# Kernel optimization log

Hardware: AMD Instinct MI355X
Metric: run time of the kernel (lower is better)

The kernel has to match this reference:

```python
import jax, jax.numpy as jnp
import numpy as np

N_NODES = 50000
N_EDGES = 800000
IN_CH = 128
EDGE_DIM = 16
N_GRAPHS = 500


def _lin_params(key, din, dout):
    k1, k2 = jax.random.split(key)
    s = 1.0 / np.sqrt(din)
    W = jax.random.uniform(k1, (din, dout), jnp.float32, -s, s)
    b = jax.random.uniform(k2, (dout,), jnp.float32, -s, s)
    return W, b


def setup_inputs() -> dict:
    key = jax.random.key(0)
    ks = jax.random.split(key, 20)
    x = jax.random.normal(ks[0], (N_NODES, IN_CH), jnp.float32)
    edge_attr = jax.random.normal(ks[1], (N_EDGES, EDGE_DIM), jnp.float32)
    edge_index = jax.random.randint(ks[2], (2, N_EDGES), 0, N_NODES, jnp.int32)
    n_nodes = jnp.full((N_GRAPHS,), N_NODES // N_GRAPHS, jnp.int32)
    inp = {"x": x, "edge_attr": edge_attr, "edge_index": edge_index, "n_nodes": n_nodes}
    # conv1: edge lin (edge_dim->128), mlp 128->256->256, bn 256
    inp["We1"], inp["be1"] = _lin_params(ks[3], EDGE_DIM, IN_CH)
    inp["W11"], inp["b11"] = _lin_params(ks[4], IN_CH, 256)
    inp["W12"], inp["b12"] = _lin_params(ks[5], 256, 256)
    inp["g1"], inp["bt1"] = jnp.ones((256,), jnp.float32), jnp.zeros((256,), jnp.float32)
    # conv2: edge lin (edge_dim->256), mlp 256->128->128, bn 128
    inp["We2"], inp["be2"] = _lin_params(ks[6], EDGE_DIM, 256)
    inp["W21"], inp["b21"] = _lin_params(ks[7], 256, 128)
    inp["W22"], inp["b22"] = _lin_params(ks[8], 128, 128)
    inp["g2"], inp["bt2"] = jnp.ones((128,), jnp.float32), jnp.zeros((128,), jnp.float32)
    # conv3: edge lin (edge_dim->128), mlp 128->64->64, bn 64
    inp["We3"], inp["be3"] = _lin_params(ks[9], EDGE_DIM, 128)
    inp["W31"], inp["b31"] = _lin_params(ks[10], 128, 64)
    inp["W32"], inp["b32"] = _lin_params(ks[11], 64, 64)
    inp["g3"], inp["bt3"] = jnp.ones((64,), jnp.float32), jnp.zeros((64,), jnp.float32)
    # head
    inp["Wf1"], inp["bf1"] = _lin_params(ks[12], 64, 16)
    inp["Wf2"], inp["bf2"] = _lin_params(ks[13], 16, 1)
    return inp


def _gine(x, src, dst, ea_proj, W1, b1, W2, b2):
    # message: relu(x_j + lin(edge_attr)); aggregate: scatter-add; GIN0 eps=0
    m = jax.nn.relu(x[src] + ea_proj)                      # [E, D]
    agg = jax.ops.segment_sum(m, dst, num_segments=N_NODES)
    h = x + agg
    return jax.nn.relu(h @ W1 + b1) @ W2 + b2


def _bn(x, g, b):
    mu = x.mean(axis=0)
    var = x.var(axis=0)
    return (x - mu) * jax.lax.rsqrt(var + 1e-5) * g + b


def reference(x, edge_attr, edge_index, n_nodes,
              We1, be1, W11, b11, W12, b12, g1, bt1,
              We2, be2, W21, b21, W22, b22, g2, bt2,
              We3, be3, W31, b31, W32, b32, g3, bt3,
              Wf1, bf1, Wf2, bf2):
    src, dst = edge_index[0], edge_index[1]
    h = _gine(x, src, dst, edge_attr @ We1 + be1, W11, b11, W12, b12)
    h = _bn(jax.nn.relu(h), g1, bt1)
    h = _gine(h, src, dst, edge_attr @ We2 + be2, W21, b21, W22, b22)
    h = _bn(jax.nn.relu(h), g2, bt2)
    h = _gine(h, src, dst, edge_attr @ We3 + be3, W31, b31, W32, b32)
    h = _bn(jax.nn.relu(h), g3, bt3)
    last_idx = jnp.cumsum(n_nodes) - 1                      # [G]
    master = h[last_idx]                                    # [G, 64]; dropout = identity (eval)
    out = jax.nn.relu(master @ Wf1 + bf1) @ Wf2 + bf2       # [G, 1]
    return out
```

## Files before the change

### kernel.cpp

```cpp
#include <hip/hip_runtime.h>
#include <hip/hip_bf16.h>


typedef __attribute__((ext_vector_type(8))) short short8;
typedef __attribute__((ext_vector_type(4))) float floatx4;
typedef __attribute__((ext_vector_type(2))) float float2v;
typedef unsigned long long u64;

__device__ __forceinline__ float2v splat2(float s) {
    float2v v; v[0] = s; v[1] = s; return v;
}

__device__ __forceinline__ int uni(int x) {
    return __builtin_amdgcn_readfirstlane(x);
}

__device__ __forceinline__ float2v pkfma_lo(u64 s, float2v w, float2v p) {
    asm("v_pk_fma_f32 %0, %1, %2, %0 op_sel:[0,0,0] op_sel_hi:[0,1,1]"
        : "+v"(p) : "s"(s), "v"(w));
    return p;
}

__device__ __forceinline__ float2v pkfma_hi(u64 s, float2v w, float2v p) {
    asm("v_pk_fma_f32 %0, %1, %2, %0 op_sel:[1,0,0] op_sel_hi:[1,1,1]"
        : "+v"(p) : "s"(s), "v"(w));
    return p;
}

__device__ __forceinline__ ushort f2bf_rne(float x) {
    unsigned u = __float_as_uint(x);
    unsigned r = (u + 0x7FFFu + ((u >> 16) & 1u)) >> 16;
    return (ushort)r;
}

__device__ __forceinline__ float bf2f(ushort u) {
    return __uint_as_float(((unsigned)u) << 16);
}


__global__ __launch_bounds__(256) void hist_kernel(const int* __restrict__ dst,
                                                   int* __restrict__ deg, int E) {
    int i = blockIdx.x * blockDim.x + threadIdx.x;
    int stride = gridDim.x * blockDim.x;
    for (; i < E; i += stride) atomicAdd(&deg[dst[i]], 1);
}

__global__ __launch_bounds__(1024) void scan_kernel(const int* __restrict__ deg,
                                                    int* __restrict__ row_start, int N) {
    __shared__ int part[1024];
    int tid = threadIdx.x;
    int per = (N + 1023) / 1024;
    int start = tid * per;
    int end = min(start + per, N);
    int s = 0;
    for (int i = start; i < end; ++i) s += deg[i];
    part[tid] = s;
    __syncthreads();
    if (tid == 0) {
        int t = 0;
        for (int i = 0; i < 1024; ++i) {
            int v = part[i];
            part[i] = t;
            t += v;
        }
    }
    __syncthreads();
    int run = part[tid];
    for (int i = start; i < end; ++i) {
        row_start[i] = run;
        run += deg[i];
    }
    if (tid == 1023) row_start[N] = run;
}

__global__ __launch_bounds__(256) void scatter_kernel(
    const int* __restrict__ src, const int* __restrict__ dst,
    const int* __restrict__ row_start, int* __restrict__ cursor,
    int2* __restrict__ csr, int E) {
    int i = blockIdx.x * blockDim.x + threadIdx.x;
    int stride = gridDim.x * blockDim.x;
    for (; i < E; i += stride) {
        int v = dst[i];
        int p = row_start[v] + atomicAdd(&cursor[v], 1);
        csr[p] = make_int2(i, src[i]);
    }
}

__device__ __forceinline__ void wsplit(const float* W, ushort* Wth, ushort* Wtl,
                                       int K, int N, int t) {
    int k = t / N, n = t - k * N;
    float v = W[t];
    ushort hv = f2bf_rne(v);
    float hf = bf2f(hv);
    ushort lv = f2bf_rne(v - hf);
    Wth[(size_t)n * K + k] = hv;
    Wtl[(size_t)n * K + k] = lv;
}

__global__ __launch_bounds__(256) void prep_all(
    const float* W11, ushort* W11h, ushort* W11l,
    const float* W12, ushort* W12h, ushort* W12l,
    const float* W21, ushort* W21h, ushort* W21l,
    const float* W22, ushort* W22h, ushort* W22l,
    const float* W31, ushort* W31h, ushort* W31l,
    const float* W32, ushort* W32h, ushort* W32l) {
    int t = blockIdx.x * blockDim.x + threadIdx.x;
    const int s1 = 128 * 256, s2 = s1 + 256 * 256, s3 = s2 + 256 * 128;
    const int s4 = s3 + 128 * 128, s5 = s4 + 128 * 64, s6 = s5 + 64 * 64;
    if (t < s1) wsplit(W11, W11h, W11l, 128, 256, t);
    else if (t < s2) wsplit(W12, W12h, W12l, 256, 256, t - s1);
    else if (t < s3) wsplit(W21, W21h, W21l, 256, 128, t - s2);
    else if (t < s4) wsplit(W22, W22h, W22l, 128, 128, t - s3);
    else if (t < s5) wsplit(W31, W31h, W31l, 128, 64, t - s4);
    else if (t < s6) wsplit(W32, W32h, W32l, 64, 64, t - s5);
}

__global__ __launch_bounds__(256) void f32_to_bf16(const float* __restrict__ in,
                                                   ushort* __restrict__ out, long n4) {
    long i = (long)blockIdx.x * blockDim.x + threadIdx.x;
    long stride = (long)gridDim.x * blockDim.x;
    for (; i < n4; i += stride) {
        float4 v = ((const float4*)in)[i];
        ushort4 o;
        o.x = f2bf_rne(v.x);
        o.y = f2bf_rne(v.y);
        o.z = f2bf_rne(v.z);
        o.w = f2bf_rne(v.w);
        ((ushort4*)out)[i] = o;
    }
}

__device__ __forceinline__ float2v edge_accum(
    const float* __restrict__ ea, int eid, unsigned rv,
    const float2v* w, float2v bias, float2v acc, float2v z2) {
    const u64* q = (const u64*)(ea + (size_t)eid * 16);
    float2v p = bias;
#pragma unroll
    for (int t = 0; t < 8; ++t) {
        u64 qt = q[t];
        p = pkfma_lo(qt, w[2 * t], p);
        p = pkfma_hi(qt, w[2 * t + 1], p);
    }
    float2v hv;
    hv[0] = __uint_as_float(rv << 16);
    hv[1] = __uint_as_float(rv & 0xffff0000u);
    float2v m = p + hv;
    return acc + __builtin_elementwise_max(m, z2);
}

template <int D, int WPN>
__global__ __launch_bounds__(256) void gine_agg_kernel(
    const float* __restrict__ h, const ushort* __restrict__ hb,
    const float* __restrict__ ea,
    const int* __restrict__ row_start, const int2* __restrict__ csr,
    const float* __restrict__ We, const float* __restrict__ be,
    ushort* __restrict__ uhi, ushort* __restrict__ ulo, int N) {
    constexpr int NPB = 4 / WPN;
    const int lane = threadIdx.x & 63;
    const int wid = threadIdx.x >> 6;
    const int ch0 = (wid % WPN) * 128 + lane * 2;

    float2v w[16];
#pragma unroll
    for (int k = 0; k < 16; ++k) w[k] = *(const float2v*)&We[k * D + ch0];
    const float2v bias = *(const float2v*)&be[ch0];

    int v = blockIdx.x * NPB + wid / WPN;
    const int vstride = gridDim.x * NPB;
    const float2v z2 = splat2(0.f);

    for (; v < N; v += vstride) {
        const int vs = uni(v);
        const int e0 = uni(row_start[vs]);
        const int e1 = uni(row_start[vs + 1]);
        float2v acc = z2;

        int i = e0;
        int rem = e1 - e0;
        if (rem >= 4) {
            int2 c0 = csr[i], c1 = csr[i + 1], c2 = csr[i + 2], c3 = csr[i + 3];
            do {
                const int ni = (rem >= 8) ? i + 4 : i;
                int2 n0 = csr[ni], n1 = csr[ni + 1];
                int2 n2 = csr[ni + 2], n3 = csr[ni + 3];

                const int sA = uni(c0.y), sB = uni(c1.y);
                const int sC = uni(c2.y), sD = uni(c3.y);
                const int eA = uni(c0.x), eB = uni(c1.x);
                const int eC = uni(c2.x), eD = uni(c3.x);

                unsigned rA = *(const unsigned*)&hb[(size_t)sA * D + ch0];
                unsigned rB = *(const unsigned*)&hb[(size_t)sB * D + ch0];
                unsigned rC = *(const unsigned*)&hb[(size_t)sC * D + ch0];
                unsigned rD = *(const unsigned*)&hb[(size_t)sD * D + ch0];

                acc = edge_accum(ea, eA, rA, w, bias, acc, z2);
                acc = edge_accum(ea, eB, rB, w, bias, acc, z2);
                acc = edge_accum(ea, eC, rC, w, bias, acc, z2);
                acc = edge_accum(ea, eD, rD, w, bias, acc, z2);

                c0 = n0; c1 = n1; c2 = n2; c3 = n3;
                i += 4;
                rem -= 4;
            } while (rem >= 4);
        }
        for (; rem > 0; --rem, ++i) {
            int2 ce = csr[i];
            const int se = uni(ce.y);
            const int ee = uni(ce.x);
            unsigned rv = *(const unsigned*)&hb[(size_t)se * D + ch0];
            acc = edge_accum(ea, ee, rv, w, bias, acc, z2);
        }
        float2v sv = *(const float2v*)&h[(size_t)v * D + ch0];
        float u0 = sv[0] + acc[0];
        float u1 = sv[1] + acc[1];
        ushort h0 = f2bf_rne(u0);
        ushort h1 = f2bf_rne(u1);
        ushort l0 = f2bf_rne(u0 - bf2f(h0));
        ushort l1 = f2bf_rne(u1 - bf2f(h1));
        *(ushort2*)&uhi[(size_t)v * D + ch0] = make_ushort2(h0, h1);
        *(ushort2*)&ulo[(size_t)v * D + ch0] = make_ushort2(l0, l1);
    }
}

template <int WRITE_BF16, int STATS>
__global__ __launch_bounds__(256) void gemm_mfma(
    const ushort* __restrict__ Ah, const ushort* __restrict__ Al,
    const ushort* __restrict__ Bh, const ushort* __restrict__ Bl,
    const float* __restrict__ bias,
    float* __restrict__ Cf, ushort* __restrict__ Chi, ushort* __restrict__ Clo,
    float* __restrict__ stats, int Nreal,
    int N, int K, int relu) {
    __shared__ ushort sA[2][128][72];
    __shared__ ushort sB[2][64][72];
    const int tid = threadIdx.x;
    const int wave = tid >> 6, lane = tid & 63;
    const int lrow = lane & 15, lquad = lane >> 4;
    const int bm = blockIdx.y * 128;
    const int bn = blockIdx.x * 64;

    floatx4 acc[2][4];
#pragma unroll
    for (int i = 0; i < 2; ++i)
#pragma unroll
        for (int j = 0; j < 4; ++j) acc[i][j] = (floatx4)0.f;

    for (int k0 = 0; k0 < K; k0 += 64) {
        for (int s = tid; s < 1024; s += 256) {
            int row = s >> 3, c8 = (s & 7) * 8;
            size_t g = (size_t)(bm + row) * K + k0 + c8;
            *(int4*)&sA[0][row][c8] = *(const int4*)&Ah[g];
            *(int4*)&sA[1][row][c8] = *(const int4*)&Al[g];
        }
        for (int s = tid; s < 512; s += 256) {
            int row = s >> 3, c8 = (s & 7) * 8;
            size_t g = (size_t)(bn + row) * K + k0 + c8;
            *(int4*)&sB[0][row][c8] = *(const int4*)&Bh[g];
            *(int4*)&sB[1][row][c8] = *(const int4*)&Bl[g];
        }
        __syncthreads();
        const int rb = wave * 32;
#pragma unroll
        for (int kk = 0; kk < 2; ++kk) {
            int ko = kk * 32 + lquad * 8;
            short8 ah[2], al[2], bh[4], bl[4];
#pragma unroll
            for (int i = 0; i < 2; ++i) {
                ah[i] = *(const short8*)&sA[0][rb + i * 16 + lrow][ko];
                al[i] = *(const short8*)&sA[1][rb + i * 16 + lrow][ko];
            }
#pragma unroll
            for (int j = 0; j < 4; ++j) {
                bh[j] = *(const short8*)&sB[0][j * 16 + lrow][ko];
                bl[j] = *(const short8*)&sB[1][j * 16 + lrow][ko];
            }
#pragma unroll
            for (int i = 0; i < 2; ++i)
#pragma unroll
                for (int j = 0; j < 4; ++j) {
                    acc[i][j] = __builtin_amdgcn_mfma_f32_16x16x32_bf16(
                        ah[i], bh[j], acc[i][j], 0, 0, 0);
                    acc[i][j] = __builtin_amdgcn_mfma_f32_16x16x32_bf16(
                        ah[i], bl[j], acc[i][j], 0, 0, 0);
                    acc[i][j] = __builtin_amdgcn_mfma_f32_16x16x32_bf16(
                        al[i], bh[j], acc[i][j], 0, 0, 0);
                }
        }
        __syncthreads();
    }
    float sj[4] = {0.f, 0.f, 0.f, 0.f};
    float qj[4] = {0.f, 0.f, 0.f, 0.f};
#pragma unroll
    for (int i = 0; i < 2; ++i)
#pragma unroll
        for (int j = 0; j < 4; ++j) {
            int gc = bn + j * 16 + lrow;
            float bv = bias[gc];
#pragma unroll
            for (int r = 0; r < 4; ++r) {
                int gr = bm + wave * 32 + i * 16 + lquad * 4 + r;
                float v = acc[i][j][r] + bv;
                if (relu) v = fmaxf(v, 0.f);
                if (STATS && gr < Nreal) {
                    sj[j] += v;
                    qj[j] = fmaf(v, v, qj[j]);
                }
                if (WRITE_BF16) {
                    ushort hv = f2bf_rne(v);
                    ushort lv = f2bf_rne(v - bf2f(hv));
                    Chi[(size_t)gr * N + gc] = hv;
                    Clo[(size_t)gr * N + gc] = lv;
                } else {
                    Cf[(size_t)gr * N + gc] = v;
                }
            }
        }
    if (STATS) {
#pragma unroll
        for (int j = 0; j < 4; ++j) {
            float s = sj[j], q = qj[j];
            s += __shfl_xor(s, 16);
            s += __shfl_xor(s, 32);
            q += __shfl_xor(q, 16);
            q += __shfl_xor(q, 32);
            if (lquad == 0) {
                int gc = bn + j * 16 + lrow;
                atomicAdd(&stats[gc], s);
                atomicAdd(&stats[N + gc], q);
            }
        }
    }
}

__global__ __launch_bounds__(256) void bn_apply_kernel(
    const float* __restrict__ r, float* __restrict__ h,
    ushort* __restrict__ hbout,
    const float* __restrict__ sums,
    const float* __restrict__ g, const float* __restrict__ bt,
    int N, int D, int Dm1) {
    int idx = blockIdx.x * blockDim.x + threadIdx.x;
    int total4 = N * D / 4;
    int stride = gridDim.x * blockDim.x;
    float invN = 1.0f / (float)N;
    for (; idx < total4; idx += stride) {
        int c = (idx * 4) & Dm1;
        float4 s4 = *(const float4*)&sums[c];
        float4 q4 = *(const float4*)&sums[D + c];
        float4 g4 = *(const float4*)&g[c];
        float4 b4 = *(const float4*)&bt[c];
        float4 r4 = ((const float4*)r)[idx];
        float4 o;
        {
            float mu = s4.x * invN;
            float var = fmaf(-mu, mu, q4.x * invN);
            o.x = (r4.x - mu) * (rsqrtf(var + 1e-5f) * g4.x) + b4.x;
            mu = s4.y * invN;
            var = fmaf(-mu, mu, q4.y * invN);
            o.y = (r4.y - mu) * (rsqrtf(var + 1e-5f) * g4.y) + b4.y;
            mu = s4.z * invN;
            var = fmaf(-mu, mu, q4.z * invN);
            o.z = (r4.z - mu) * (rsqrtf(var + 1e-5f) * g4.z) + b4.z;
            mu = s4.w * invN;
            var = fmaf(-mu, mu, q4.w * invN);
            o.w = (r4.w - mu) * (rsqrtf(var + 1e-5f) * g4.w) + b4.w;
        }
        ((float4*)h)[idx] = o;
        if (hbout) {
            ushort4 ob;
            ob.x = f2bf_rne(o.x);
            ob.y = f2bf_rne(o.y);
            ob.z = f2bf_rne(o.z);
            ob.w = f2bf_rne(o.w);
            ((ushort4*)hbout)[idx] = ob;
        }
    }
}

__global__ void head_kernel(const float* __restrict__ h, const int* __restrict__ n_nodes,
                            const float* __restrict__ Wf1, const float* __restrict__ bf1,
                            const float* __restrict__ Wf2, const float* __restrict__ bf2,
                            float* __restrict__ out, int G) {
    int g = blockIdx.x * blockDim.x + threadIdx.x;
    if (g >= G) return;
    int s = 0;
    for (int i = 0; i <= g; ++i) s += n_nodes[i];
    const float* m = &h[(size_t)(s - 1) * 64];
    float o = bf2[0];
#pragma unroll 4
    for (int j = 0; j < 16; ++j) {
        float acc = bf1[j];
        for (int k = 0; k < 64; ++k) acc = fmaf(m[k], Wf1[k * 16 + j], acc);
        acc = fmaxf(acc, 0.f);
        o = fmaf(acc, Wf2[j], o);
    }
    out[g] = o;
}

extern "C" void kernel_launch(void* const* d_in, const int* in_sizes, int n_in,
                              void* d_out, int out_size, void* d_ws, size_t ws_size,
                              hipStream_t stream) {
    const float* x = (const float*)d_in[0];
    const float* ea = (const float*)d_in[1];
    const int* eidx = (const int*)d_in[2];
    const int* n_nodes = (const int*)d_in[3];
    const float* We1 = (const float*)d_in[4];
    const float* be1 = (const float*)d_in[5];
    const float* W11 = (const float*)d_in[6];
    const float* b11 = (const float*)d_in[7];
    const float* W12 = (const float*)d_in[8];
    const float* b12 = (const float*)d_in[9];
    const float* g1 = (const float*)d_in[10];
    const float* bt1 = (const float*)d_in[11];
    const float* We2 = (const float*)d_in[12];
    const float* be2 = (const float*)d_in[13];
    const float* W21 = (const float*)d_in[14];
    const float* b21 = (const float*)d_in[15];
    const float* W22 = (const float*)d_in[16];
    const float* b22 = (const float*)d_in[17];
    const float* g2 = (const float*)d_in[18];
    const float* bt2 = (const float*)d_in[19];
    const float* We3 = (const float*)d_in[20];
    const float* be3 = (const float*)d_in[21];
    const float* W31 = (const float*)d_in[22];
    const float* b31 = (const float*)d_in[23];
    const float* W32 = (const float*)d_in[24];
    const float* b32 = (const float*)d_in[25];
    const float* g3 = (const float*)d_in[26];
    const float* bt3 = (const float*)d_in[27];
    const float* Wf1 = (const float*)d_in[28];
    const float* bf1 = (const float*)d_in[29];
    const float* Wf2 = (const float*)d_in[30];
    const float* bf2 = (const float*)d_in[31];

    const int N = in_sizes[0] / 128;
    const int E = in_sizes[2] / 2;
    const int G = in_sizes[3];
    const int Mp = ((N + 127) / 128) * 128;
    const int* srcp = eidx;
    const int* dstp = eidx + E;

    float* H = (float*)d_ws;
    float* UR = H + (size_t)Mp * 256;
    float* TT = UR + (size_t)Mp * 256;
    float* stats1 = TT + (size_t)Mp * 256;
    float* stats2 = stats1 + 512;
    float* stats3 = stats2 + 256;
    int* deg = (int*)(stats3 + 128);
    int* cursor = deg + N;
    int* row_start = cursor + N;
    int2* csr = (int2*)(row_start + N + 2);
    size_t woff = (size_t)((int*)(csr + E) - (int*)d_ws);
    woff = (woff + 3) & ~(size_t)3;
    ushort* wp = (ushort*)((int*)d_ws + woff);
    ushort* W11th = wp; wp += 128 * 256;
    ushort* W11tl = wp; wp += 128 * 256;
    ushort* W12th = wp; wp += 256 * 256;
    ushort* W12tl = wp; wp += 256 * 256;
    ushort* W21th = wp; wp += 256 * 128;
    ushort* W21tl = wp; wp += 256 * 128;
    ushort* W22th = wp; wp += 128 * 128;
    ushort* W22tl = wp; wp += 128 * 128;
    ushort* W31th = wp; wp += 128 * 64;
    ushort* W31tl = wp; wp += 128 * 64;
    ushort* W32th = wp; wp += 64 * 64;
    ushort* W32tl = wp; wp += 64 * 64;

    hipMemsetAsync(stats1, 0, 896 * sizeof(float) + (size_t)2 * N * sizeof(int), stream);

    const int prepTot = 128 * 256 + 256 * 256 + 256 * 128 + 128 * 128 + 128 * 64 + 64 * 64;
    prep_all<<<(prepTot + 255) / 256, 256, 0, stream>>>(
        W11, W11th, W11tl, W12, W12th, W12tl, W21, W21th, W21tl,
        W22, W22th, W22tl, W31, W31th, W31tl, W32, W32th, W32tl);

    hist_kernel<<<3125, 256, 0, stream>>>(dstp, deg, E);
    scan_kernel<<<1, 1024, 0, stream>>>(deg, row_start, N);
    scatter_kernel<<<3125, 256, 0, stream>>>(srcp, dstp, row_start, cursor, csr, E);

    const int gy = Mp / 128;
    float* R = UR;
    ushort* HB = (ushort*)TT;

    {
        ushort* Uhi = (ushort*)UR; ushort* Ulo = Uhi + (size_t)Mp * 128;
        ushort* Thi = (ushort*)TT; ushort* Tlo = Thi + (size_t)Mp * 256;
        f32_to_bf16<<<2048, 256, 0, stream>>>(x, HB, (long)N * 128 / 4);
        gine_agg_kernel<128, 1><<<(N + 3) / 4, 256, 0, stream>>>(
            x, HB, ea, row_start, csr, We1, be1, Uhi, Ulo, N);
        gemm_mfma<1, 0><<<dim3(4, gy), 256, 0, stream>>>(
            Uhi, Ulo, W11th, W11tl, b11, nullptr, Thi, Tlo, nullptr, 0, 256, 128, 1);
        gemm_mfma<0, 1><<<dim3(4, gy), 256, 0, stream>>>(
            Thi, Tlo, W12th, W12tl, b12, R, nullptr, nullptr, stats1, N, 256, 256, 1);
        bn_apply_kernel<<<2048, 256, 0, stream>>>(R, H, HB, stats1, g1, bt1, N, 256, 255);
    }

    {
        ushort* Uhi = (ushort*)UR; ushort* Ulo = Uhi + (size_t)Mp * 256;
        ushort* Thi = (ushort*)TT; ushort* Tlo = Thi + (size_t)Mp * 128;
        gine_agg_kernel<256, 2><<<(N + 1) / 2, 256, 0, stream>>>(
            H, HB, ea, row_start, csr, We2, be2, Uhi, Ulo, N);
        gemm_mfma<1, 0><<<dim3(2, gy), 256, 0, stream>>>(
            Uhi, Ulo, W21th, W21tl, b21, nullptr, Thi, Tlo, nullptr, 0, 128, 256, 1);
        gemm_mfma<0, 1><<<dim3(2, gy), 256, 0, stream>>>(
            Thi, Tlo, W22th, W22tl, b22, R, nullptr, nullptr, stats2, N, 128, 128, 1);
        bn_apply_kernel<<<2048, 256, 0, stream>>>(R, H, HB, stats2, g2, bt2, N, 128, 127);
    }

    {
        ushort* Uhi = (ushort*)UR; ushort* Ulo = Uhi + (size_t)Mp * 128;
        ushort* Thi = (ushort*)TT; ushort* Tlo = Thi + (size_t)Mp * 64;
        gine_agg_kernel<128, 1><<<(N + 3) / 4, 256, 0, stream>>>(
            H, HB, ea, row_start, csr, We3, be3, Uhi, Ulo, N);
        gemm_mfma<1, 0><<<dim3(1, gy), 256, 0, stream>>>(
            Uhi, Ulo, W31th, W31tl, b31, nullptr, Thi, Tlo, nullptr, 0, 64, 128, 1);
        gemm_mfma<0, 1><<<dim3(1, gy), 256, 0, stream>>>(
            Thi, Tlo, W32th, W32tl, b32, R, nullptr, nullptr, stats3, N, 64, 64, 1);
        bn_apply_kernel<<<2048, 256, 0, stream>>>(R, H, nullptr, stats3, g3, bt3, N, 64, 63);
    }

    head_kernel<<<(G + 255) / 256, 256, 0, stream>>>(H, n_nodes, Wf1, bf1, Wf2, bf2,
                                                     (float*)d_out, G);
}
```

Before: 923.6 us.

## Compute per-edge projection with MFMA inside GINE aggregation using bf16-split edge attrs

Replaces the scalar packed-FMA per-edge edge_attr projection in the aggregation kernel with MFMA 16x16x32 bf16 ops. Sixteen edges are processed per step, with the gathered neighbour features fed in as the accumulator and bias folded in via a ones column. Edge attributes are converted once to hi/lo bf16 pairs, and edge weights are pre-laid out in MFMA fragment order and staged in LDS. This aims to cut the VALU cost of the 16-wide projection per edge per channel. In exchange it adds prep kernels, extra workspace, cross-lane reductions and masked tail handling. The split-bf16 precision is kept for the inputs, but neighbour features stay single bf16.

After: 1.332 ms. 44.2% more time.

```diff
diff --git a/kernel.cpp b/kernel.cpp
--- a/kernel.cpp
+++ b/kernel.cpp
@@ -4,28 +4,6 @@
 
 typedef __attribute__((ext_vector_type(8))) short short8;
 typedef __attribute__((ext_vector_type(4))) float floatx4;
-typedef __attribute__((ext_vector_type(2))) float float2v;
-typedef unsigned long long u64;
-
-__device__ __forceinline__ float2v splat2(float s) {
-    float2v v; v[0] = s; v[1] = s; return v;
-}
-
-__device__ __forceinline__ int uni(int x) {
-    return __builtin_amdgcn_readfirstlane(x);
-}
-
-__device__ __forceinline__ float2v pkfma_lo(u64 s, float2v w, float2v p) {
-    asm("v_pk_fma_f32 %0, %1, %2, %0 op_sel:[0,0,0] op_sel_hi:[0,1,1]"
-        : "+v"(p) : "s"(s), "v"(w));
-    return p;
-}
-
-__device__ __forceinline__ float2v pkfma_hi(u64 s, float2v w, float2v p) {
-    asm("v_pk_fma_f32 %0, %1, %2, %0 op_sel:[1,0,0] op_sel_hi:[1,1,1]"
-        : "+v"(p) : "s"(s), "v"(w));
-    return p;
-}
 
 __device__ __forceinline__ ushort f2bf_rne(float x) {
     unsigned u = __float_as_uint(x);
@@ -115,6 +93,79 @@
     else if (t < s6) wsplit(W32, W32h, W32l, 64, 64, t - s5);
 }
 
+__global__ __launch_bounds__(256) void prep_edgeW(
+    const float* __restrict__ We1, const float* __restrict__ be1, ushort* __restrict__ O1,
+    const float* __restrict__ We2, const float* __restrict__ be2, ushort* __restrict__ O2,
+    const float* __restrict__ We3, const float* __restrict__ be3, ushort* __restrict__ O3) {
+    int o = blockIdx.x * 256 + threadIdx.x;
+    const int L1 = 8 * 2 * 512, L2e = L1 + 16 * 2 * 512, L3e = L2e + 8 * 2 * 512;
+    const float* We;
+    const float* be;
+    ushort* out;
+    int D, local;
+    if (o < L1) { We = We1; be = be1; out = O1; D = 128; local = o; }
+    else if (o < L2e) { We = We2; be = be2; out = O2; D = 256; local = o - L1; }
+    else if (o < L3e) { We = We3; be = be3; out = O3; D = 128; local = o - L2e; }
+    else return;
+    int j = local & 7;
+    int l = (local >> 3) & 63;
+    int b = (local >> 9) & 1;
+    int t = local >> 10;
+    int kq = (l >> 4) * 8 + j;
+    int n = t * 16 + (l & 15);
+    int k = kq & 15;
+    float w = We[k * D + n];
+    ushort hv = f2bf_rne(w);
+    ushort res;
+    if (b == 0) {
+        res = hv;
+    } else {
+        if (kq < 16) {
+            res = f2bf_rne(w - bf2f(hv));
+        } else if (kq == 16) {
+            res = f2bf_rne(be[n]);
+        } else if (kq == 17) {
+            float bh = bf2f(f2bf_rne(be[n]));
+            res = f2bf_rne(be[n] - bh);
+        } else {
+            res = 0;
+        }
+    }
+    out[local] = res;
+}
+
+__global__ __launch_bounds__(256) void prep_eab(const float* __restrict__ ea,
+                                                ushort* __restrict__ eab, int E) {
+    int e = blockIdx.x * blockDim.x + threadIdx.x;
+    int stride = gridDim.x * blockDim.x;
+    for (; e < E; e += stride) {
+        const float4* p = (const float4*)(ea + (size_t)e * 16);
+        ushort hi[16], lo[16];
+#pragma unroll
+        for (int c4 = 0; c4 < 4; ++c4) {
+            float4 v = p[c4];
+            float vv[4] = {v.x, v.y, v.z, v.w};
+#pragma unroll
+            for (int r = 0; r < 4; ++r) {
+                int d = c4 * 4 + r;
+                ushort h = f2bf_rne(vv[r]);
+                hi[d] = h;
+                lo[d] = f2bf_rne(vv[r] - bf2f(h));
+            }
+        }
+        unsigned w[16];
+#pragma unroll
+        for (int d = 0; d < 8; ++d) w[d] = (unsigned)hi[2 * d] | ((unsigned)hi[2 * d + 1] << 16);
+#pragma unroll
+        for (int d = 0; d < 8; ++d) w[8 + d] = (unsigned)lo[2 * d] | ((unsigned)lo[2 * d + 1] << 16);
+        int4* o4 = (int4*)(eab + (size_t)e * 32);
+        o4[0] = make_int4(w[0], w[1], w[2], w[3]);
+        o4[1] = make_int4(w[4], w[5], w[6], w[7]);
+        o4[2] = make_int4(w[8], w[9], w[10], w[11]);
+        o4[3] = make_int4(w[12], w[13], w[14], w[15]);
+    }
+}
+
 __global__ __launch_bounds__(256) void f32_to_bf16(const float* __restrict__ in,
                                                    ushort* __restrict__ out, long n4) {
     long i = (long)blockIdx.x * blockDim.x + threadIdx.x;
@@ -130,96 +181,124 @@
     }
 }
 
-__device__ __forceinline__ float2v edge_accum(
-    const float* __restrict__ ea, int eid, unsigned rv,
-    const float2v* w, float2v bias, float2v acc, float2v z2) {
-    const u64* q = (const u64*)(ea + (size_t)eid * 16);
-    float2v p = bias;
-#pragma unroll
-    for (int t = 0; t < 8; ++t) {
-        u64 qt = q[t];
-        p = pkfma_lo(qt, w[2 * t], p);
-        p = pkfma_hi(qt, w[2 * t + 1], p);
-    }
-    float2v hv;
-    hv[0] = __uint_as_float(rv << 16);
-    hv[1] = __uint_as_float(rv & 0xffff0000u);
-    float2v m = p + hv;
-    return acc + __builtin_elementwise_max(m, z2);
-}
-
 template <int D, int WPN>
-__global__ __launch_bounds__(256) void gine_agg_kernel(
+__global__ __launch_bounds__(256) void gine_agg_mfma(
     const float* __restrict__ h, const ushort* __restrict__ hb,
-    const float* __restrict__ ea,
+    const ushort* __restrict__ eab,
     const int* __restrict__ row_start, const int2* __restrict__ csr,
-    const float* __restrict__ We, const float* __restrict__ be,
+    const ushort* __restrict__ WeB,
     ushort* __restrict__ uhi, ushort* __restrict__ ulo, int N) {
     constexpr int NPB = 4 / WPN;
-    const int lane = threadIdx.x & 63;
-    const int wid = threadIdx.x >> 6;
-    const int ch0 = (wid % WPN) * 128 + lane * 2;
-
-    float2v w[16];
-#pragma unroll
-    for (int k = 0; k < 16; ++k) w[k] = *(const float2v*)&We[k * D + ch0];
-    const float2v bias = *(const float2v*)&be[ch0];
+    constexpr int NT = D / (16 * WPN);
+    __shared__ ushort sW[(D / 16) * 2 * 512];
+
+    const int tid = threadIdx.x;
+    for (int s = tid; s < (D / 16) * 2 * 512 / 8; s += 256)
+        ((int4*)sW)[s] = ((const int4*)WeB)[s];
+    __syncthreads();
+
+    const int lane = tid & 63;
+    const int wid = tid >> 6;
+    const int n16 = lane & 15;
+    const int q = lane >> 4;
+    const int q4 = q * 4;
+    const bool hiq = q < 2;
+    const int onesx = (q == 2) ? 0x3F803F80 : 0;
+    const int chW = (wid % WPN) * 128;
+    const ushort* sWl = sW + (size_t)(chW * 64) + lane * 8;
 
     int v = blockIdx.x * NPB + wid / WPN;
     const int vstride = gridDim.x * NPB;
-    const float2v z2 = splat2(0.f);
+    const floatx4 z4 = (floatx4)0.f;
 
     for (; v < N; v += vstride) {
-        const int vs = uni(v);
-        const int e0 = uni(row_start[vs]);
-        const int e1 = uni(row_start[vs + 1]);
-        float2v acc = z2;
+        const int e0 = row_start[v];
+        const int e1 = row_start[v + 1];
+        floatx4 macc[NT];
+#pragma unroll
+        for (int t = 0; t < NT; ++t) macc[t] = z4;
+
+        auto body = [&](int2 c, int rem, bool tail) {
+            short8 a1 = *(const short8*)&eab[(size_t)c.x * 32 + q * 8];
+            int4 a1i = *reinterpret_cast<int4*>(&a1);
+            int4 a2i;
+            a2i.x = hiq ? a1i.x : onesx;
+            a2i.y = hiq ? a1i.y : 0;
+            a2i.z = hiq ? a1i.z : 0;
+            a2i.w = hiq ? a1i.w : 0;
+            short8 a2 = *reinterpret_cast<short8*>(&a2i);
+            int s0 = __shfl(c.y, q4 + 0);
+            int s1 = __shfl(c.y, q4 + 1);
+            int s2 = __shfl(c.y, q4 + 2);
+            int s3 = __shfl(c.y, q4 + 3);
+            const ushort* p0 = hb + (size_t)s0 * D + chW + n16;
+            const ushort* p1 = hb + (size_t)s1 * D + chW + n16;
+            const ushort* p2 = hb + (size_t)s2 * D + chW + n16;
+            const ushort* p3 = hb + (size_t)s3 * D + chW + n16;
+            unsigned xr0[NT], xr1[NT], xr2[NT], xr3[NT];
+#pragma unroll
+            for (int t = 0; t < NT; ++t) {
+                xr0[t] = p0[t * 16];
+                xr1[t] = p1[t * 16];
+                xr2[t] = p2[t * 16];
+                xr3[t] = p3[t * 16];
+            }
+            bool m0 = true, m1 = true, m2 = true, m3 = true;
+            if (tail) {
+                m0 = (q4 + 0) < rem;
+                m1 = (q4 + 1) < rem;
+                m2 = (q4 + 2) < rem;
+                m3 = (q4 + 3) < rem;
+            }
+#pragma unroll
+            for (int t = 0; t < NT; ++t) {
+                floatx4 acc;
+                acc[0] = __uint_as_float(xr0[t] << 16);
+                acc[1] = __uint_as_float(xr1[t] << 16);
+                acc[2] = __uint_as_float(xr2[t] << 16);
+                acc[3] = __uint_as_float(xr3[t] << 16);
+                if (tail) {
+                    acc[0] = m0 ? acc[0] : -1e30f;
+                    acc[1] = m1 ? acc[1] : -1e30f;
+                    acc[2] = m2 ? acc[2] : -1e30f;
+                    acc[3] = m3 ? acc[3] : -1e30f;
+                }
+                short8 b1 = *(const short8*)&sWl[t * 1024];
+                short8 b2 = *(const short8*)&sWl[t * 1024 + 512];
+                acc = __builtin_amdgcn_mfma_f32_16x16x32_bf16(a1, b1, acc, 0, 0, 0);
+                acc = __builtin_amdgcn_mfma_f32_16x16x32_bf16(a2, b2, acc, 0, 0, 0);
+                macc[t] += __builtin_elementwise_max(acc, z4);
+            }
+        };
 
         int i = e0;
         int rem = e1 - e0;
-        if (rem >= 4) {
-            int2 c0 = csr[i], c1 = csr[i + 1], c2 = csr[i + 2], c3 = csr[i + 3];
-            do {
-                const int ni = (rem >= 8) ? i + 4 : i;
-                int2 n0 = csr[ni], n1 = csr[ni + 1];
-                int2 n2 = csr[ni + 2], n3 = csr[ni + 3];
-
-                const int sA = uni(c0.y), sB = uni(c1.y);
-                const int sC = uni(c2.y), sD = uni(c3.y);
-                const int eA = uni(c0.x), eB = uni(c1.x);
-                const int eC = uni(c2.x), eD = uni(c3.x);
-
-                unsigned rA = *(const unsigned*)&hb[(size_t)sA * D + ch0];
-                unsigned rB = *(const unsigned*)&hb[(size_t)sB * D + ch0];
-                unsigned rC = *(const unsigned*)&hb[(size_t)sC * D + ch0];
-                unsigned rD = *(const unsigned*)&hb[(size_t)sD * D + ch0];
-
-                acc = edge_accum(ea, eA, rA, w, bias, acc, z2);
-                acc = edge_accum(ea, eB, rB, w, bias, acc, z2);
-                acc = edge_accum(ea, eC, rC, w, bias, acc, z2);
-                acc = edge_accum(ea, eD, rD, w, bias, acc, z2);
-
-                c0 = n0; c1 = n1; c2 = n2; c3 = n3;
-                i += 4;
-                rem -= 4;
-            } while (rem >= 4);
-        }
-        for (; rem > 0; --rem, ++i) {
-            int2 ce = csr[i];
-            const int se = uni(ce.y);
-            const int ee = uni(ce.x);
-            unsigned rv = *(const unsigned*)&hb[(size_t)se * D + ch0];
-            acc = edge_accum(ea, ee, rv, w, bias, acc, z2);
-        }
-        float2v sv = *(const float2v*)&h[(size_t)v * D + ch0];
-        float u0 = sv[0] + acc[0];
-        float u1 = sv[1] + acc[1];
-        ushort h0 = f2bf_rne(u0);
-        ushort h1 = f2bf_rne(u1);
-        ushort l0 = f2bf_rne(u0 - bf2f(h0));
-        ushort l1 = f2bf_rne(u1 - bf2f(h1));
-        *(ushort2*)&uhi[(size_t)v * D + ch0] = make_ushort2(h0, h1);
-        *(ushort2*)&ulo[(size_t)v * D + ch0] = make_ushort2(l0, l1);
+        if (rem > 0) {
+            int2 c = csr[i + min(n16, rem - 1)];
+            while (rem > 16) {
+                int2 cn = csr[i + 16 + min(n16, rem - 17)];
+                body(c, 16, false);
+                c = cn;
+                i += 16;
+                rem -= 16;
+            }
+            body(c, rem, rem < 16);
+        }
+
+#pragma unroll
+        for (int t = 0; t < NT; ++t) {
+            float s = macc[t][0] + macc[t][1] + macc[t][2] + macc[t][3];
+            s += __shfl_xor(s, 16);
+            s += __shfl_xor(s, 32);
+            if (q == (t & 3)) {
+                int ch = chW + t * 16 + n16;
+                float u = h[(size_t)v * D + ch] + s;
+                ushort h0 = f2bf_rne(u);
+                ushort l0 = f2bf_rne(u - bf2f(h0));
+                uhi[(size_t)v * D + ch] = h0;
+                ulo[(size_t)v * D + ch] = l0;
+            }
+        }
     }
 }
 
@@ -464,6 +543,15 @@
     ushort* W31tl = wp; wp += 128 * 64;
     ushort* W32th = wp; wp += 64 * 64;
     ushort* W32tl = wp; wp += 64 * 64;
+    ushort* WeB1 = wp; wp += 8 * 2 * 512;
+    ushort* WeB2 = wp; wp += 16 * 2 * 512;
+    ushort* WeB3 = wp; wp += 8 * 2 * 512;
+    {
+        size_t off = (size_t)(wp - (ushort*)d_ws);
+        off = (off + 7) & ~(size_t)7;
+        wp = (ushort*)d_ws + off;
+    }
+    ushort* eab = wp;
 
     hipMemsetAsync(stats1, 0, 896 * sizeof(float) + (size_t)2 * N * sizeof(int), stream);
 
@@ -471,6 +559,9 @@
     prep_all<<<(prepTot + 255) / 256, 256, 0, stream>>>(
         W11, W11th, W11tl, W12, W12th, W12tl, W21, W21th, W21tl,
         W22, W22th, W22tl, W31, W31th, W31tl, W32, W32th, W32tl);
+    prep_edgeW<<<(32 * 2 * 512 + 255) / 256, 256, 0, stream>>>(
+        We1, be1, WeB1, We2, be2, WeB2, We3, be3, WeB3);
+    prep_eab<<<3125, 256, 0, stream>>>(ea, eab, E);
 
     hist_kernel<<<3125, 256, 0, stream>>>(dstp, deg, E);
     scan_kernel<<<1, 1024, 0, stream>>>(deg, row_start, N);
@@ -484,8 +575,8 @@
         ushort* Uhi = (ushort*)UR; ushort* Ulo = Uhi + (size_t)Mp * 128;
         ushort* Thi = (ushort*)TT; ushort* Tlo = Thi + (size_t)Mp * 256;
         f32_to_bf16<<<2048, 256, 0, stream>>>(x, HB, (long)N * 128 / 4);
-        gine_agg_kernel<128, 1><<<(N + 3) / 4, 256, 0, stream>>>(
-            x, HB, ea, row_start, csr, We1, be1, Uhi, Ulo, N);
+        gine_agg_mfma<128, 1><<<(N + 3) / 4, 256, 0, stream>>>(
+            x, HB, eab, row_start, csr, WeB1, Uhi, Ulo, N);
         gemm_mfma<1, 0><<<dim3(4, gy), 256, 0, stream>>>(
             Uhi, Ulo, W11th, W11tl, b11, nullptr, Thi, Tlo, nullptr, 0, 256, 128, 1);
         gemm_mfma<0, 1><<<dim3(4, gy), 256, 0, stream>>>(
@@ -496,8 +587,8 @@
     {
         ushort* Uhi = (ushort*)UR; ushort* Ulo = Uhi + (size_t)Mp * 256;
         ushort* Thi = (ushort*)TT; ushort* Tlo = Thi + (size_t)Mp * 128;
-        gine_agg_kernel<256, 2><<<(N + 1) / 2, 256, 0, stream>>>(
-            H, HB, ea, row_start, csr, We2, be2, Uhi, Ulo, N);
+        gine_agg_mfma<256, 2><<<(N + 1) / 2, 256, 0, stream>>>(
+            H, HB, eab, row_start, csr, WeB2, Uhi, Ulo, N);
         gemm_mfma<1, 0><<<dim3(2, gy), 256, 0, stream>>>(
             Uhi, Ulo, W21th, W21tl, b21, nullptr, Thi, Tlo, nullptr, 0, 128, 256, 1);
         gemm_mfma<0, 1><<<dim3(2, gy), 256, 0, stream>>>(
@@ -508,8 +599,8 @@
     {
         ushort* Uhi = (ushort*)UR; ushort* Ulo = Uhi + (size_t)Mp * 128;
         ushort* Thi = (ushort*)TT; ushort* Tlo = Thi + (size_t)Mp * 64;
-        gine_agg_kernel<128, 1><<<(N + 3) / 4, 256, 0, stream>>>(
-            H, HB, ea, row_start, csr, We3, be3, Uhi, Ulo, N);
+        gine_agg_mfma<128, 1><<<(N + 3) / 4, 256, 0, stream>>>(
+            H, HB, eab, row_start, csr, WeB3, Uhi, Ulo, N);
         gemm_mfma<1, 0><<<dim3(1, gy), 256, 0, stream>>>(
             Uhi, Ulo, W31th, W31tl, b31, nullptr, Thi, Tlo, nullptr, 0, 64, 128, 1);
         gemm_mfma<0, 1><<<dim3(1, gy), 256, 0, stream>>>(
```

## Permute edge attributes into CSR order and software-pipeline edge loop

Applied to the files above, without the earlier changes.

Splits the CSR into separate edge-id and source arrays and adds a gather kernel that copies edge_attr into CSR (destination-sorted) order once, so the three aggregation passes stream edge features contiguously instead of gathering them by random edge id. The aggregation kernel drops the grid-stride loop and readfirstlane scalarization, and uses a two-deep manual prefetch of edge features, source index and source row. Edge features now live in VGPRs instead of SGPRs, which raises register pressure. The change also adds a 51 MB extra workspace buffer and one extra gather pass.

Measured after the change: 1.294 ms. 1.4x slower.

```diff
diff --git a/kernel.cpp b/kernel.cpp
--- a/kernel.cpp
+++ b/kernel.cpp
@@ -7,23 +7,15 @@
 typedef __attribute__((ext_vector_type(2))) float float2v;
 typedef unsigned long long u64;
 
-__device__ __forceinline__ float2v splat2(float s) {
-    float2v v; v[0] = s; v[1] = s; return v;
-}
-
-__device__ __forceinline__ int uni(int x) {
-    return __builtin_amdgcn_readfirstlane(x);
-}
-
-__device__ __forceinline__ float2v pkfma_lo(u64 s, float2v w, float2v p) {
+__device__ __forceinline__ float2v pkfma_lo(u64 e, float2v w, float2v p) {
     asm("v_pk_fma_f32 %0, %1, %2, %0 op_sel:[0,0,0] op_sel_hi:[0,1,1]"
-        : "+v"(p) : "s"(s), "v"(w));
+        : "+v"(p) : "v"(e), "v"(w));
     return p;
 }
 
-__device__ __forceinline__ float2v pkfma_hi(u64 s, float2v w, float2v p) {
+__device__ __forceinline__ float2v pkfma_hi(u64 e, float2v w, float2v p) {
     asm("v_pk_fma_f32 %0, %1, %2, %0 op_sel:[1,0,0] op_sel_hi:[1,1,1]"
-        : "+v"(p) : "s"(s), "v"(w));
+        : "+v"(p) : "v"(e), "v"(w));
     return p;
 }
 
@@ -76,13 +68,26 @@
 __global__ __launch_bounds__(256) void scatter_kernel(
     const int* __restrict__ src, const int* __restrict__ dst,
     const int* __restrict__ row_start, int* __restrict__ cursor,
-    int2* __restrict__ csr, int E) {
+    int* __restrict__ ceid, int* __restrict__ csrc, int E) {
     int i = blockIdx.x * blockDim.x + threadIdx.x;
     int stride = gridDim.x * blockDim.x;
     for (; i < E; i += stride) {
         int v = dst[i];
         int p = row_start[v] + atomicAdd(&cursor[v], 1);
-        csr[p] = make_int2(i, src[i]);
+        ceid[p] = i;
+        csrc[p] = src[i];
+    }
+}
+
+__global__ __launch_bounds__(256) void eacsr_gather(const float* __restrict__ ea,
+                                                    const int* __restrict__ ceid,
+                                                    float* __restrict__ eacsr, long total) {
+    long t = (long)blockIdx.x * 256 + threadIdx.x;
+    long stride = (long)gridDim.x * 256;
+    for (; t < total; t += stride) {
+        long p = t >> 4;
+        int c = (int)(t & 15);
+        eacsr[t] = ea[(size_t)ceid[p] * 16 + c];
     }
 }
 
@@ -130,29 +135,11 @@
     }
 }
 
-__device__ __forceinline__ float2v edge_accum(
-    const float* __restrict__ ea, int eid, unsigned rv,
-    const float2v* w, float2v bias, float2v acc, float2v z2) {
-    const u64* q = (const u64*)(ea + (size_t)eid * 16);
-    float2v p = bias;
-#pragma unroll
-    for (int t = 0; t < 8; ++t) {
-        u64 qt = q[t];
-        p = pkfma_lo(qt, w[2 * t], p);
-        p = pkfma_hi(qt, w[2 * t + 1], p);
-    }
-    float2v hv;
-    hv[0] = __uint_as_float(rv << 16);
-    hv[1] = __uint_as_float(rv & 0xffff0000u);
-    float2v m = p + hv;
-    return acc + __builtin_elementwise_max(m, z2);
-}
-
 template <int D, int WPN>
 __global__ __launch_bounds__(256) void gine_agg_kernel(
     const float* __restrict__ h, const ushort* __restrict__ hb,
-    const float* __restrict__ ea,
-    const int* __restrict__ row_start, const int2* __restrict__ csr,
+    const float* __restrict__ eacsr,
+    const int* __restrict__ row_start, const int* __restrict__ csrc,
     const float* __restrict__ We, const float* __restrict__ be,
     ushort* __restrict__ uhi, ushort* __restrict__ ulo, int N) {
     constexpr int NPB = 4 / WPN;
@@ -165,62 +152,77 @@
     for (int k = 0; k < 16; ++k) w[k] = *(const float2v*)&We[k * D + ch0];
     const float2v bias = *(const float2v*)&be[ch0];
 
-    int v = blockIdx.x * NPB + wid / WPN;
-    const int vstride = gridDim.x * NPB;
-    const float2v z2 = splat2(0.f);
-
-    for (; v < N; v += vstride) {
-        const int vs = uni(v);
-        const int e0 = uni(row_start[vs]);
-        const int e1 = uni(row_start[vs + 1]);
-        float2v acc = z2;
-
+    const int v = blockIdx.x * NPB + wid / WPN;
+    if (v >= N) return;
+    float2v z2; z2[0] = 0.f; z2[1] = 0.f;
+
+    const int e0 = row_start[v];
+    const int e1 = row_start[v + 1];
+    float2v acc = z2;
+
+#define LOADEA(B0, B1, B2, B3, B4, B5, B6, B7, idx)                  \
+    {                                                                \
+        const u64* q_ = (const u64*)eacsr + (size_t)(idx) * 8;       \
+        B0 = q_[0]; B1 = q_[1]; B2 = q_[2]; B3 = q_[3];              \
+        B4 = q_[4]; B5 = q_[5]; B6 = q_[6]; B7 = q_[7];              \
+    }
+
+#define COMP(B0, B1, B2, B3, B4, B5, B6, B7, r)                      \
+    {                                                                \
+        float2v p = bias;                                            \
+        p = pkfma_lo(B0, w[0], p);  p = pkfma_hi(B0, w[1], p);       \
+        p = pkfma_lo(B1, w[2], p);  p = pkfma_hi(B1, w[3], p);       \
+        p = pkfma_lo(B2, w[4], p);  p = pkfma_hi(B2, w[5], p);       \
+        p = pkfma_lo(B3, w[6], p);  p = pkfma_hi(B3, w[7], p);       \
+        p = pkfma_lo(B4, w[8], p);  p = pkfma_hi(B4, w[9], p);       \
+        p = pkfma_lo(B5, w[10], p); p = pkfma_hi(B5, w[11], p);      \
+        p = pkfma_lo(B6, w[12], p); p = pkfma_hi(B6, w[13], p);      \
+        float2v hv;                                                  \
+        hv[0] = __uint_as_float((r) << 16);                          \
+        hv[1] = __uint_as_float((r) & 0xffff0000u);                  \
+        p = pkfma_lo(B7, w[14], p); p = pkfma_hi(B7, w[15], p);      \
+        float2v m = p + hv;                                          \
+        acc += __builtin_elementwise_max(m, z2);                     \
+    }
+
+    if (e1 > e0) {
         int i = e0;
-        int rem = e1 - e0;
-        if (rem >= 4) {
-            int2 c0 = csr[i], c1 = csr[i + 1], c2 = csr[i + 2], c3 = csr[i + 3];
-            do {
-                const int ni = (rem >= 8) ? i + 4 : i;
-                int2 n0 = csr[ni], n1 = csr[ni + 1];
-                int2 n2 = csr[ni + 2], n3 = csr[ni + 3];
-
-                const int sA = uni(c0.y), sB = uni(c1.y);
-                const int sC = uni(c2.y), sD = uni(c3.y);
-                const int eA = uni(c0.x), eB = uni(c1.x);
-                const int eC = uni(c2.x), eD = uni(c3.x);
-
-                unsigned rA = *(const unsigned*)&hb[(size_t)sA * D + ch0];
-                unsigned rB = *(const unsigned*)&hb[(size_t)sB * D + ch0];
-                unsigned rC = *(const unsigned*)&hb[(size_t)sC * D + ch0];
-                unsigned rD = *(const unsigned*)&hb[(size_t)sD * D + ch0];
-
-                acc = edge_accum(ea, eA, rA, w, bias, acc, z2);
-                acc = edge_accum(ea, eB, rB, w, bias, acc, z2);
-                acc = edge_accum(ea, eC, rC, w, bias, acc, z2);
-                acc = edge_accum(ea, eD, rD, w, bias, acc, z2);
-
-                c0 = n0; c1 = n1; c2 = n2; c3 = n3;
-                i += 4;
-                rem -= 4;
-            } while (rem >= 4);
-        }
-        for (; rem > 0; --rem, ++i) {
-            int2 ce = csr[i];
-            const int se = uni(ce.y);
-            const int ee = uni(ce.x);
-            unsigned rv = *(const unsigned*)&hb[(size_t)se * D + ch0];
-            acc = edge_accum(ea, ee, rv, w, bias, acc, z2);
-        }
-        float2v sv = *(const float2v*)&h[(size_t)v * D + ch0];
-        float u0 = sv[0] + acc[0];
-        float u1 = sv[1] + acc[1];
-        ushort h0 = f2bf_rne(u0);
-        ushort h1 = f2bf_rne(u1);
-        ushort l0 = f2bf_rne(u0 - bf2f(h0));
-        ushort l1 = f2bf_rne(u1 - bf2f(h1));
-        *(ushort2*)&uhi[(size_t)v * D + ch0] = make_ushort2(h0, h1);
-        *(ushort2*)&ulo[(size_t)v * D + ch0] = make_ushort2(l0, l1);
-    }
+        u64 A0, A1, A2, A3, A4, A5, A6, A7;
+        u64 B0, B1, B2, B3, B4, B5, B6, B7;
+        int s0 = csrc[i];
+        LOADEA(A0, A1, A2, A3, A4, A5, A6, A7, i);
+        unsigned rA = *(const unsigned*)&hb[(size_t)s0 * D + ch0];
+        int s1 = csrc[i + 1];
+        while (i + 2 < e1) {
+            LOADEA(B0, B1, B2, B3, B4, B5, B6, B7, i + 1);
+            unsigned rB = *(const unsigned*)&hb[(size_t)s1 * D + ch0];
+            int s2 = csrc[i + 2];
+            COMP(A0, A1, A2, A3, A4, A5, A6, A7, rA);
+            LOADEA(A0, A1, A2, A3, A4, A5, A6, A7, i + 2);
+            rA = *(const unsigned*)&hb[(size_t)s2 * D + ch0];
+            s1 = csrc[i + 3];
+            COMP(B0, B1, B2, B3, B4, B5, B6, B7, rB);
+            i += 2;
+        }
+        COMP(A0, A1, A2, A3, A4, A5, A6, A7, rA);
+        if (i + 1 < e1) {
+            LOADEA(B0, B1, B2, B3, B4, B5, B6, B7, i + 1);
+            unsigned rB = *(const unsigned*)&hb[(size_t)s1 * D + ch0];
+            COMP(B0, B1, B2, B3, B4, B5, B6, B7, rB);
+        }
+    }
+#undef LOADEA
+#undef COMP
+
+    float2v sv = *(const float2v*)&h[(size_t)v * D + ch0];
+    float u0 = sv[0] + acc[0];
+    float u1 = sv[1] + acc[1];
+    ushort h0 = f2bf_rne(u0);
+    ushort h1 = f2bf_rne(u1);
+    ushort l0 = f2bf_rne(u0 - bf2f(h0));
+    ushort l1 = f2bf_rne(u1 - bf2f(h1));
+    *(ushort2*)&uhi[(size_t)v * D + ch0] = make_ushort2(h0, h1);
+    *(ushort2*)&ulo[(size_t)v * D + ch0] = make_ushort2(l0, l1);
 }
 
 template <int WRITE_BF16, int STATS>
@@ -448,10 +450,9 @@
     int* deg = (int*)(stats3 + 128);
     int* cursor = deg + N;
     int* row_start = cursor + N;
-    int2* csr = (int2*)(row_start + N + 2);
-    size_t woff = (size_t)((int*)(csr + E) - (int*)d_ws);
-    woff = (woff + 3) & ~(size_t)3;
-    ushort* wp = (ushort*)((int*)d_ws + woff);
+    int* ceid = row_start + N + 2;
+    int* csrc = ceid + E;
+    ushort* wp = (ushort*)(csrc + E + 2);
     ushort* W11th = wp; wp += 128 * 256;
     ushort* W11tl = wp; wp += 128 * 256;
     ushort* W12th = wp; wp += 256 * 256;
@@ -464,6 +465,12 @@
     ushort* W31tl = wp; wp += 128 * 64;
     ushort* W32th = wp; wp += 64 * 64;
     ushort* W32tl = wp; wp += 64 * 64;
+    float* eacsr;
+    {
+        size_t off = (size_t)((char*)wp - (char*)d_ws);
+        off = (off + 15) & ~(size_t)15;
+        eacsr = (float*)((char*)d_ws + off);
+    }
 
     hipMemsetAsync(stats1, 0, 896 * sizeof(float) + (size_t)2 * N * sizeof(int), stream);
 
@@ -474,7 +481,8 @@
 
     hist_kernel<<<3125, 256, 0, stream>>>(dstp, deg, E);
     scan_kernel<<<1, 1024, 0, stream>>>(deg, row_start, N);
-    scatter_kernel<<<3125, 256, 0, stream>>>(srcp, dstp, row_start, cursor, csr, E);
+    scatter_kernel<<<3125, 256, 0, stream>>>(srcp, dstp, row_start, cursor, ceid, csrc, E);
+    eacsr_gather<<<12500, 256, 0, stream>>>(ea, ceid, eacsr, (long)E * 16);
 
     const int gy = Mp / 128;
     float* R = UR;
@@ -485,7 +493,7 @@
         ushort* Thi = (ushort*)TT; ushort* Tlo = Thi + (size_t)Mp * 256;
         f32_to_bf16<<<2048, 256, 0, stream>>>(x, HB, (long)N * 128 / 4);
         gine_agg_kernel<128, 1><<<(N + 3) / 4, 256, 0, stream>>>(
-            x, HB, ea, row_start, csr, We1, be1, Uhi, Ulo, N);
+            x, HB, eacsr, row_start, csrc, We1, be1, Uhi, Ulo, N);
         gemm_mfma<1, 0><<<dim3(4, gy), 256, 0, stream>>>(
             Uhi, Ulo, W11th, W11tl, b11, nullptr, Thi, Tlo, nullptr, 0, 256, 128, 1);
         gemm_mfma<0, 1><<<dim3(4, gy), 256, 0, stream>>>(
@@ -497,7 +505,7 @@
         ushort* Uhi = (ushort*)UR; ushort* Ulo = Uhi + (size_t)Mp * 256;
         ushort* Thi = (ushort*)TT; ushort* Tlo = Thi + (size_t)Mp * 128;
         gine_agg_kernel<256, 2><<<(N + 1) / 2, 256, 0, stream>>>(
-            H, HB, ea, row_start, csr, We2, be2, Uhi, Ulo, N);
+            H, HB, eacsr, row_start, csrc, We2, be2, Uhi, Ulo, N);
         gemm_mfma<1, 0><<<dim3(2, gy), 256, 0, stream>>>(
             Uhi, Ulo, W21th, W21tl, b21, nullptr, Thi, Tlo, nullptr, 0, 128, 256, 1);
         gemm_mfma<0, 1><<<dim3(2, gy), 256, 0, stream>>>(
@@ -509,7 +517,7 @@
         ushort* Uhi = (ushort*)UR; ushort* Ulo = Uhi + (size_t)Mp * 128;
         ushort* Thi = (ushort*)TT; ushort* Tlo = Thi + (size_t)Mp * 64;
         gine_agg_kernel<128, 1><<<(N + 3) / 4, 256, 0, stream>>>(
-            H, HB, ea, row_start, csr, We3, be3, Uhi, Ulo, N);
+            H, HB, eacsr, row_start, csrc, We3, be3, Uhi, Ulo, N);
         gemm_mfma<1, 0><<<dim3(1, gy), 256, 0, stream>>>(
             Uhi, Ulo, W31th, W31tl, b31, nullptr, Thi, Tlo, nullptr, 0, 64, 128, 1);
         gemm_mfma<0, 1><<<dim3(1, gy), 256, 0, stream>>>(
```
